# Performance work log

Hardware: AMD Instinct MI355X
Metric: run time of the kernel (lower is better)

## Reference

```python
import jax, jax.numpy as jnp
import numpy as np

ZONEOUT = 0.1
OUT_CHANNELS = 80
REDUCTION_FACTOR = 2


def setup_inputs() -> dict:
    key = jax.random.key(0)
    ks = jax.random.split(key, 7)
    B, H, T, L = 64, 1024, 500, 2
    s = 1.0 / np.sqrt(H)
    return {
        "res_output": jax.random.normal(ks[0], (B, H, T), dtype=jnp.float32),
        "Wih": jax.random.normal(ks[1], (L, 3 * H, H), dtype=jnp.float32) * s,
        "Whh": jax.random.normal(ks[2], (L, 3 * H, H), dtype=jnp.float32) * s,
        "bih": jax.random.normal(ks[3], (L, 3 * H), dtype=jnp.float32) * s,
        "bhh": jax.random.normal(ks[4], (L, 3 * H), dtype=jnp.float32) * s,
        "Wout": jax.random.normal(ks[5], (OUT_CHANNELS * 2, H), dtype=jnp.float32) * s,
        "bout": jax.random.normal(ks[6], (OUT_CHANNELS * 2,), dtype=jnp.float32) * s,
    }


def _gru_cell(x, h, wih, whh, bi, bh):
    # torch.nn.GRUCell math
    gi = x @ wih.T + bi            # (B, 3H)
    gh = h @ whh.T + bh            # (B, 3H)
    i_r, i_z, i_n = jnp.split(gi, 3, axis=-1)
    h_r, h_z, h_n = jnp.split(gh, 3, axis=-1)
    r = jax.nn.sigmoid(i_r + h_r)
    z = jax.nn.sigmoid(i_z + h_z)
    n = jnp.tanh(i_n + r * h_n)
    return (1.0 - z) * n + z * h


def reference(res_output, Wih, Whh, bih, bhh, Wout, bout):
    B, H, T = res_output.shape
    L = Wih.shape[0]
    xs = jnp.transpose(res_output, (2, 0, 1))  # (T, B, H)

    def step(hs, x):
        new_hs = []
        inp = x
        for l in range(L):  # static small layer loop
            h_new = _gru_cell(inp, hs[l], Wih[l], Whh[l], bih[l], bhh[l])
            # eval-mode zoneout: deterministic blend
            h_new = ZONEOUT * hs[l] + (1.0 - ZONEOUT) * h_new
            new_hs.append(h_new)
            inp = h_new
        y = inp @ Wout.T + bout  # (B, 2*out_channels)
        return tuple(new_hs), y

    h0 = tuple(jnp.zeros((B, H), dtype=res_output.dtype) for _ in range(L))
    _, ys = jax.lax.scan(step, h0, xs)  # (T, B, 2*oc)
    ys = ys.reshape(T, B, OUT_CHANNELS, REDUCTION_FACTOR)
    # concat per-step (B, oc, rf) blocks along last dim -> (B, oc, T*rf)
    out = jnp.transpose(ys, (1, 2, 0, 3)).reshape(B, OUT_CHANNELS, T * REDUCTION_FACTOR)
    return out
```

## Files before the change

kernel.cpp:

```cpp
#include <hip/hip_runtime.h>

typedef __attribute__((ext_vector_type(8))) short bhalf8;
typedef __attribute__((ext_vector_type(4))) float floatx4;

#define NSLOTS 502
#define NWG 128
#define BLOCK 768

#define AS1 __attribute__((address_space(1)))
#define AS3 __attribute__((address_space(3)))
#define GLL_COH(g, s)   __builtin_amdgcn_global_load_lds((const AS1 unsigned*)(g), (AS3 unsigned*)(s), 16, 0, 17)
#define GLL_PLAIN(g, s) __builtin_amdgcn_global_load_lds((const AS1 unsigned*)(g), (AS3 unsigned*)(s), 16, 0, 0)

__device__ __forceinline__ unsigned short f2b(float f) {
  unsigned u = __float_as_uint(f);
  return (unsigned short)((u + 0x7FFFu + ((u >> 16) & 1u)) >> 16);
}
__device__ __forceinline__ int cloadi(const int* p) {
  return __hip_atomic_load(p, __ATOMIC_RELAXED, __HIP_MEMORY_SCOPE_AGENT);
}
__device__ __forceinline__ void cstorei(int* p, int v) {
  __hip_atomic_store(p, v, __ATOMIC_RELAXED, __HIP_MEMORY_SCOPE_AGENT);
}
__device__ __forceinline__ void cstore(unsigned long long* p, unsigned long long v) {
  __hip_atomic_store(p, v, __ATOMIC_RELAXED, __HIP_MEMORY_SCOPE_AGENT);
}

__global__ void prep_w(const float* __restrict__ wih, const float* __restrict__ whh,
                       const float* __restrict__ wout,
                       unsigned short* __restrict__ wihb, unsigned short* __restrict__ whhb,
                       unsigned short* __restrict__ woutb) {
  size_t i0 = (size_t)blockIdx.x * blockDim.x + threadIdx.x;
  size_t stride = (size_t)gridDim.x * blockDim.x;
  for (size_t i = i0; i < 6291456u; i += stride) { wihb[i] = f2b(wih[i]); whhb[i] = f2b(whh[i]); }
  for (size_t i = i0; i < 163840u; i += stride) woutb[i] = f2b(wout[i]);
}

__global__ void prep_x(const float* __restrict__ x, unsigned short* __restrict__ xb) {
  __shared__ float tile[32][33];
  int b = blockIdx.z;
  int h0 = blockIdx.y * 32, t0 = blockIdx.x * 32;
  int tx = threadIdx.x, ty = threadIdx.y;
  #pragma unroll
  for (int i = 0; i < 32; i += 8) {
    int t = t0 + tx;
    if (t < 500) tile[ty + i][tx] = x[((size_t)b * 1024 + h0 + ty + i) * 500 + t];
  }
  __syncthreads();
  #pragma unroll
  for (int i = 0; i < 32; i += 8) {
    int t = t0 + ty + i;
    if (t < 500) xb[((size_t)t * 64 + b) * 1024 + h0 + tx] = f2b(tile[tx][ty + i]);
  }
}


__launch_bounds__(BLOCK, 3)
__global__ void gru_main(const unsigned short* __restrict__ xb,
                         const unsigned short* __restrict__ wihb,
                         const unsigned short* __restrict__ whhb,
                         const unsigned short* __restrict__ woutb,
                         const float* __restrict__ bih, const float* __restrict__ bhh,
                         const float* __restrict__ bout,
                         char* __restrict__ wsb, float* __restrict__ out) {
  int* flg = (int*)wsb;
  char* h0p[3] = { wsb + 1024, wsb + 132096, wsb + 263168 };
  char* h1p[2] = { wsb + 394240, wsb + 525312 };

  const int wg = blockIdx.x;
  const int layer = wg >> 6;
  const int sub = wg & 63;
  const int eta = sub >> 5;
  const int c = sub & 31;
  const int n0c = c * 32;
  const int rb = eta * 32;
  const int tid = threadIdx.x;
  const int w = tid >> 6;
  const int l = tid & 63;
  const int l15 = l & 15, l4 = l >> 4;
  const int sd = w / 6;
  const int g = (w % 6) >> 1;
  const int u = w & 1;

  __shared__ __align__(16) char smem[131072];

  const unsigned short* Wsd = (sd ? whhb : wihb) + (size_t)layer * 3145728;
  const unsigned short* wrow = Wsd + (size_t)(g * 1024 + n0c + u * 16 + l15) * 1024 + l4 * 8;

  float bir[3][4], bhr[3][4];
  {
    int j0 = (tid & 7) << 2;
    #pragma unroll
    for (int q = 0; q < 4; ++q)
      #pragma unroll
      for (int gg = 0; gg < 3; ++gg) {
        bir[gg][q] = bih[layer * 3072 + gg * 1024 + n0c + j0 + q];
        bhr[gg][q] = bhh[layer * 3072 + gg * 1024 + n0c + j0 + q];
      }
  }
  float hcr[4] = {0.f, 0.f, 0.f, 0.f};
  int dead = 0;

  for (int s = 0; s < NSLOTS; ++s) {
    if (layer == 0) {
      if (s <= 499) {
        const char* xsrc = (const char*)xb + (size_t)s * 131072 + (size_t)rb * 2048;
        #pragma unroll
        for (int i = 0; i < 6; ++i) {
          int idx = w + i * 12;
          if (idx < 64) {
            int row = idx >> 1, hh = idx & 1;
            GLL_PLAIN(xsrc + row * 2048 + ((hh * 1024 + l * 16) ^ ((row & 7) << 4)),
                      smem + idx * 1024);
          }
        }
        if (w == 0 && !dead) {
          int it = 0;
          for (;;) {
            int f0 = cloadi(&flg[l]);
            int f1 = cloadi(&flg[64 + l]);
            if (__all(f0 >= s && f1 >= s - 1)) break;
            __builtin_amdgcn_s_sleep(1);
            if (++it > 500000) { dead = 1; break; }
          }
        }
        asm volatile("s_waitcnt vmcnt(0)" ::: "memory");
        __builtin_amdgcn_s_barrier();
        __builtin_amdgcn_sched_barrier(0);
        const char* h0src = h0p[(s + 2) % 3] + (size_t)rb * 2048;
        #pragma unroll
        for (int i = 0; i < 6; ++i) {
          int idx = w + i * 12;
          if (idx < 64) {
            int row = idx >> 1, hh = idx & 1;
            GLL_COH(h0src + row * 2048 + ((hh * 1024 + l * 16) ^ ((row & 7) << 4)),
                    smem + 65536 + idx * 1024);
          }
        }
        asm volatile("s_waitcnt vmcnt(0)" ::: "memory");
        __builtin_amdgcn_s_barrier();
        __builtin_amdgcn_sched_barrier(0);
        const char* Ab = smem + sd * 65536;
        floatx4 acc[2];
        acc[0] = (floatx4){0.f, 0.f, 0.f, 0.f};
        acc[1] = (floatx4){0.f, 0.f, 0.f, 0.f};
        #pragma unroll
        for (int ks = 0; ks < 32; ++ks) {
          bhalf8 bb = *(const bhalf8*)(wrow + ks * 32);
          #pragma unroll
          for (int m = 0; m < 2; ++m) {
            int row = m * 16 + l15;
            bhalf8 a = *(const bhalf8*)(Ab + row * 2048 + ((ks * 64 + l4 * 16) ^ ((row & 7) << 4)));
            acc[m] = __builtin_amdgcn_mfma_f32_16x16x32_bf16(a, bb, acc[m], 0, 0, 0);
          }
        }
        __syncthreads();
        float* Gsf = (float*)smem;
        #pragma unroll
        for (int m = 0; m < 2; ++m)
          #pragma unroll
          for (int i = 0; i < 4; ++i)
            Gsf[w * 576 + (m * 16 + l4 * 4 + i) * 18 + l15] = acc[m][i];
        __syncthreads();
        if (tid < 256) {
          int lr = tid >> 3, j0 = (tid & 7) << 2;
          char* hout = h0p[s % 3];
          union { unsigned long long ull; unsigned short us[4]; } pk;
          #pragma unroll
          for (int q = 0; q < 4; ++q) {
            int j = j0 + q, u_ = j >> 4, jj = j & 15;
            float ir  = Gsf[(0 + u_) * 576 + lr * 18 + jj] + bir[0][q];
            float iz  = Gsf[(2 + u_) * 576 + lr * 18 + jj] + bir[1][q];
            float inn = Gsf[(4 + u_) * 576 + lr * 18 + jj] + bir[2][q];
            float hr  = Gsf[(6 + u_) * 576 + lr * 18 + jj] + bhr[0][q];
            float hz  = Gsf[(8 + u_) * 576 + lr * 18 + jj] + bhr[1][q];
            float hn  = Gsf[(10 + u_) * 576 + lr * 18 + jj] + bhr[2][q];
            float rg = 1.f / (1.f + expf(-(ir + hr)));
            float zg = 1.f / (1.f + expf(-(iz + hz)));
            float nc = tanhf(inn + rg * hn);
            float hp = hcr[q];
            float hnew = (1.f - zg) * nc + zg * hp;
            float hzo = 0.1f * hp + 0.9f * hnew;
            hcr[q] = hzo;
            pk.us[q] = f2b(hzo);
          }
          cstore((unsigned long long*)(hout + (size_t)(rb + lr) * 2048 + ((n0c + j0) << 1)), pk.ull);
        }
      }
      __syncthreads();
      if (tid == 0) cstorei(&flg[wg], s + 1);
    } else {
      const bool gemm = (s >= 1 && s <= 500);
      if (s >= 1) {
        if (w == 0 && !dead) {
          int it = 0;
          for (;;) {
            int f0 = cloadi(&flg[l]);
            int f1 = cloadi(&flg[64 + l]);
            if (__all(f0 >= s && f1 >= s)) break;
            __builtin_amdgcn_s_sleep(1);
            if (++it > 500000) { dead = 1; break; }
          }
        }
        __builtin_amdgcn_s_barrier();
        __builtin_amdgcn_sched_barrier(0);
        const char* h0src = h0p[(s + 2) % 3] + (size_t)rb * 2048;
        const char* h1src = h1p[s & 1] + (size_t)rb * 2048;
        if (gemm) {
          #pragma unroll
          for (int i = 0; i < 11; ++i) {
            int idx = w + i * 12;
            if (idx < 128) {
              int pl = idx >> 6, r6 = idx & 63;
              int row = r6 >> 1, hh = r6 & 1;
              GLL_COH((pl ? h1src : h0src) + row * 2048 + ((hh * 1024 + l * 16) ^ ((row & 7) << 4)),
                      smem + pl * 65536 + r6 * 1024);
            }
          }
        } else {
          #pragma unroll
          for (int i = 0; i < 6; ++i) {
            int idx = w + i * 12;
            if (idx < 64) {
              int row = idx >> 1, hh = idx & 1;
              GLL_COH(h1src + row * 2048 + ((hh * 1024 + l * 16) ^ ((row & 7) << 4)),
                      smem + 65536 + idx * 1024);
            }
          }
        }
        asm volatile("s_waitcnt vmcnt(0)" ::: "memory");
        __builtin_amdgcn_s_barrier();
        __builtin_amdgcn_sched_barrier(0);
        floatx4 acc[2];
        acc[0] = (floatx4){0.f, 0.f, 0.f, 0.f};
        acc[1] = (floatx4){0.f, 0.f, 0.f, 0.f};
        if (gemm) {
          const char* Ab = smem + sd * 65536;
          #pragma unroll
          for (int ks = 0; ks < 32; ++ks) {
            bhalf8 bb = *(const bhalf8*)(wrow + ks * 32);
            #pragma unroll
            for (int m = 0; m < 2; ++m) {
              int row = m * 16 + l15;
              bhalf8 a = *(const bhalf8*)(Ab + row * 2048 + ((ks * 64 + l4 * 16) ^ ((row & 7) << 4)));
              acc[m] = __builtin_amdgcn_mfma_f32_16x16x32_bf16(a, bb, acc[m], 0, 0, 0);
            }
          }
        }
        if (s >= 2 && c < 5 && w < 2) {
          int t2 = s - 2;
          #pragma unroll
          for (int nt = 0; nt < 2; ++nt) {
            int col = c * 32 + nt * 16 + l15;
            const unsigned short* brow = woutb + (size_t)col * 1024 + l4 * 8;
            floatx4 accy = (floatx4){0.f, 0.f, 0.f, 0.f};
            #pragma unroll
            for (int ks = 0; ks < 32; ++ks) {
              int row = w * 16 + l15;
              bhalf8 a = *(const bhalf8*)(smem + 65536 + row * 2048 +
                         ((ks * 64 + l4 * 16) ^ ((row & 7) << 4)));
              bhalf8 bb = *(const bhalf8*)(brow + ks * 32);
              accy = __builtin_amdgcn_mfma_f32_16x16x32_bf16(a, bb, accy, 0, 0, 0);
            }
            float bo = bout[col];
            #pragma unroll
            for (int i = 0; i < 4; ++i) {
              int b = rb + w * 16 + l4 * 4 + i;
              out[(size_t)b * 80000 + (size_t)(col >> 1) * 1000 + t2 * 2 + (col & 1)] = accy[i] + bo;
            }
          }
        }
        if (gemm) {
          __syncthreads();
          float* Gsf = (float*)smem;
          #pragma unroll
          for (int m = 0; m < 2; ++m)
            #pragma unroll
            for (int i = 0; i < 4; ++i)
              Gsf[w * 576 + (m * 16 + l4 * 4 + i) * 18 + l15] = acc[m][i];
          __syncthreads();
          if (tid < 256) {
            int lr = tid >> 3, j0 = (tid & 7) << 2;
            char* hout = h1p[(s & 1) ^ 1];
            union { unsigned long long ull; unsigned short us[4]; } pk;
            #pragma unroll
            for (int q = 0; q < 4; ++q) {
              int j = j0 + q, u_ = j >> 4, jj = j & 15;
              float ir  = Gsf[(0 + u_) * 576 + lr * 18 + jj] + bir[0][q];
              float iz  = Gsf[(2 + u_) * 576 + lr * 18 + jj] + bir[1][q];
              float inn = Gsf[(4 + u_) * 576 + lr * 18 + jj] + bir[2][q];
              float hr  = Gsf[(6 + u_) * 576 + lr * 18 + jj] + bhr[0][q];
              float hz  = Gsf[(8 + u_) * 576 + lr * 18 + jj] + bhr[1][q];
              float hn  = Gsf[(10 + u_) * 576 + lr * 18 + jj] + bhr[2][q];
              float rg = 1.f / (1.f + expf(-(ir + hr)));
              float zg = 1.f / (1.f + expf(-(iz + hz)));
              float nc = tanhf(inn + rg * hn);
              float hp = hcr[q];
              float hnew = (1.f - zg) * nc + zg * hp;
              float hzo = 0.1f * hp + 0.9f * hnew;
              hcr[q] = hzo;
              pk.us[q] = f2b(hzo);
            }
            cstore((unsigned long long*)(hout + (size_t)(rb + lr) * 2048 + ((n0c + j0) << 1)), pk.ull);
          }
        }
      }
      __syncthreads();
      if (tid == 0) cstorei(&flg[wg], s + 1);
    }
  }
}

extern "C" void kernel_launch(void* const* d_in, const int* in_sizes, int n_in,
                              void* d_out, int out_size, void* d_ws, size_t ws_size,
                              hipStream_t stream) {
  const float* res  = (const float*)d_in[0];
  const float* Wih  = (const float*)d_in[1];
  const float* Whh  = (const float*)d_in[2];
  const float* bih  = (const float*)d_in[3];
  const float* bhh  = (const float*)d_in[4];
  const float* Wout = (const float*)d_in[5];
  const float* bout = (const float*)d_in[6];
  float* out = (float*)d_out;
  char* ws = (char*)d_ws;
  if (ws_size < 91685888u) return;

  unsigned short* woutb = (unsigned short*)(ws + 656384);
  unsigned short* wihb  = (unsigned short*)(ws + 984064);
  unsigned short* whhb  = (unsigned short*)(ws + 13566976);
  unsigned short* xb    = (unsigned short*)(ws + 26149888);

  hipMemsetAsync(ws, 0, 656384, stream);
  prep_w<<<4096, 256, 0, stream>>>(Wih, Whh, Wout, wihb, whhb, woutb);
  prep_x<<<dim3(16, 32, 64), dim3(32, 8), 0, stream>>>(res, xb);
  gru_main<<<NWG, BLOCK, 0, stream>>>(xb, wihb, whhb, woutb, bih, bhh, bout, ws, out);
}
```

Baseline: 15.89 ms.

## Pin GRU layers to separate XCDs with XCC-local hidden-state exchange

Launches 256 workgroups and uses the hardware XCC ID with an atomic counter to assign 32 workgroups on XCD 0 to layer 0 and 32 on XCD 1 to layer 1, exiting the rest. Each workgroup now handles all 64 batch rows with a K-split across waves. Hidden state stays within one XCD through plain stores and SC0 loads, and layer-0 output crosses to layer 1 through a remote buffer that layer 1 copies locally each step behind an extra flag barrier. The aim is to cut cross-XCD coherent traffic on the serial recurrence. In exchange it adds a copy-and-sync stage, converts Wout from fp32 inline on every step, and depends on enough workgroups landing on XCDs 0 and 1.

```diff
diff --git a/kernel.cpp b/kernel.cpp
--- a/kernel.cpp
+++ b/kernel.cpp
@@ -4,12 +4,11 @@
 typedef __attribute__((ext_vector_type(4))) float floatx4;
 
 #define NSLOTS 502
-#define NWG 128
 #define BLOCK 768
 
 #define AS1 __attribute__((address_space(1)))
 #define AS3 __attribute__((address_space(3)))
-#define GLL_COH(g, s)   __builtin_amdgcn_global_load_lds((const AS1 unsigned*)(g), (AS3 unsigned*)(s), 16, 0, 17)
+#define GLL_SC0(g, s)   __builtin_amdgcn_global_load_lds((const AS1 unsigned*)(g), (AS3 unsigned*)(s), 16, 0, 1)
 #define GLL_PLAIN(g, s) __builtin_amdgcn_global_load_lds((const AS1 unsigned*)(g), (AS3 unsigned*)(s), 16, 0, 0)
 
 __device__ __forceinline__ unsigned short f2b(float f) {
@@ -22,18 +21,18 @@
 __device__ __forceinline__ void cstorei(int* p, int v) {
   __hip_atomic_store(p, v, __ATOMIC_RELAXED, __HIP_MEMORY_SCOPE_AGENT);
 }
-__device__ __forceinline__ void cstore(unsigned long long* p, unsigned long long v) {
+__device__ __forceinline__ unsigned long long cload8(const unsigned long long* p) {
+  return __hip_atomic_load(p, __ATOMIC_RELAXED, __HIP_MEMORY_SCOPE_AGENT);
+}
+__device__ __forceinline__ void cstore8(unsigned long long* p, unsigned long long v) {
   __hip_atomic_store(p, v, __ATOMIC_RELAXED, __HIP_MEMORY_SCOPE_AGENT);
 }
 
 __global__ void prep_w(const float* __restrict__ wih, const float* __restrict__ whh,
-                       const float* __restrict__ wout,
-                       unsigned short* __restrict__ wihb, unsigned short* __restrict__ whhb,
-                       unsigned short* __restrict__ woutb) {
+                       unsigned short* __restrict__ wihb, unsigned short* __restrict__ whhb) {
   size_t i0 = (size_t)blockIdx.x * blockDim.x + threadIdx.x;
   size_t stride = (size_t)gridDim.x * blockDim.x;
   for (size_t i = i0; i < 6291456u; i += stride) { wihb[i] = f2b(wih[i]); whhb[i] = f2b(whh[i]); }
-  for (size_t i = i0; i < 163840u; i += stride) woutb[i] = f2b(wout[i]);
 }
 
 __global__ void prep_x(const float* __restrict__ x, unsigned short* __restrict__ xb) {
@@ -55,37 +54,56 @@
 }
 
 
-__launch_bounds__(BLOCK, 3)
+__launch_bounds__(BLOCK, 1)
 __global__ void gru_main(const unsigned short* __restrict__ xb,
                          const unsigned short* __restrict__ wihb,
                          const unsigned short* __restrict__ whhb,
-                         const unsigned short* __restrict__ woutb,
+                         const float* __restrict__ wout,
                          const float* __restrict__ bih, const float* __restrict__ bhh,
                          const float* __restrict__ bout,
                          char* __restrict__ wsb, float* __restrict__ out) {
-  int* flg = (int*)wsb;
-  char* h0p[3] = { wsb + 1024, wsb + 132096, wsb + 263168 };
-  char* h1p[2] = { wsb + 394240, wsb + 525312 };
-
-  const int wg = blockIdx.x;
-  const int layer = wg >> 6;
-  const int sub = wg & 63;
-  const int eta = sub >> 5;
-  const int c = sub & 31;
-  const int n0c = c * 32;
-  const int rb = eta * 32;
+  int* flgL0rem = (int*)wsb;
+  int* flgL1rem = (int*)(wsb + 128);
+  int* flgCopy  = (int*)(wsb + 384);
+  int* xcdcnt   = (int*)(wsb + 512);
+  char* h0rem  = wsb + 1024;
+  char* h1loc  = wsb + 263168;
+  char* h0loc0 = wsb + 525312;
+  char* h0loc1 = wsb + 787456;
+
   const int tid = threadIdx.x;
   const int w = tid >> 6;
   const int l = tid & 63;
   const int l15 = l & 15, l4 = l >> 4;
-  const int sd = w / 6;
-  const int g = (w % 6) >> 1;
-  const int u = w & 1;
+  const int g = w >> 2;
+  const int u = (w >> 1) & 1;
+  const int kh = w & 1;
 
   __shared__ __align__(16) char smem[131072];
-
-  const unsigned short* Wsd = (sd ? whhb : wihb) + (size_t)layer * 3145728;
-  const unsigned short* wrow = Wsd + (size_t)(g * 1024 + n0c + u * 16 + l15) * 1024 + l4 * 8;
+  __shared__ int role_sh;
+
+  unsigned xcc;
+  asm volatile("s_getreg_b32 %0, hwreg(HW_REG_XCC_ID)" : "=s"(xcc));
+  xcc &= 7u;
+  if (tid == 0) {
+    int rank = __hip_atomic_fetch_add(&xcdcnt[xcc], 1, __ATOMIC_RELAXED, __HIP_MEMORY_SCOPE_AGENT);
+    int role = -1;
+    if (xcc == 0 && rank < 32) role = rank;
+    else if (xcc == 1 && rank < 32) role = 32 + rank;
+    role_sh = role;
+  }
+  __syncthreads();
+  const int role = role_sh;
+  if (role < 0) return;
+
+  const int layer = (role < 32) ? 0 : 1;
+  const int c = (layer == 0) ? role : role - 32;
+  const int n0c = c * 32;
+
+  const unsigned short* wrowA = wihb + (size_t)layer * 3145728 +
+      (size_t)(g * 1024 + n0c + u * 16 + l15) * 1024 + kh * 512 + l4 * 8;
+  const unsigned short* wrowB = whhb + (size_t)layer * 3145728 +
+      (size_t)(g * 1024 + n0c + u * 16 + l15) * 1024 + kh * 512 + l4 * 8;
 
   float bir[3][4], bhr[3][4];
   {
@@ -101,80 +119,92 @@
   float hcr[4] = {0.f, 0.f, 0.f, 0.f};
   int dead = 0;
 
-  for (int s = 0; s < NSLOTS; ++s) {
-    if (layer == 0) {
+  auto gather = [&](const char* src, int sc0) {
+    #pragma unroll
+    for (int i = 0; i < 11; ++i) {
+      int idx = w + i * 12;
+      if (idx < 128) {
+        int row = idx >> 1, hh = idx & 1;
+        const char* ga = src + row * 2048 + ((hh * 1024 + l * 16) ^ ((row & 7) << 4));
+        if (sc0) GLL_SC0(ga, smem + idx * 1024); else GLL_PLAIN(ga, smem + idx * 1024);
+      }
+    }
+  };
+  auto gemm = [&](const unsigned short* wrow, floatx4* acc) {
+    #pragma unroll
+    for (int ks = 0; ks < 16; ++ks) {
+      bhalf8 bb = *(const bhalf8*)(wrow + ks * 32);
+      #pragma unroll
+      for (int m = 0; m < 4; ++m) {
+        int row = m * 16 + l15;
+        bhalf8 a = *(const bhalf8*)(smem + row * 2048 +
+                   ((kh * 1024 + ks * 64 + l4 * 16) ^ ((row & 7) << 4)));
+        acc[m] = __builtin_amdgcn_mfma_f32_16x16x32_bf16(a, bb, acc[m], 0, 0, 0);
+      }
+    }
+  };
+  auto dumpGs = [&](floatx4* acc, int sideofs) {
+    float* Gsf = (float*)smem;
+    #pragma unroll
+    for (int m = 0; m < 4; ++m)
+      #pragma unroll
+      for (int i = 0; i < 4; ++i)
+        Gsf[(sideofs + w) * 1088 + (m * 16 + l4 * 4 + i) * 17 + l15] = acc[m][i];
+  };
+
+  if (layer == 0) {
+    for (int s = 0; s < NSLOTS; ++s) {
       if (s <= 499) {
-        const char* xsrc = (const char*)xb + (size_t)s * 131072 + (size_t)rb * 2048;
-        #pragma unroll
-        for (int i = 0; i < 6; ++i) {
-          int idx = w + i * 12;
-          if (idx < 64) {
-            int row = idx >> 1, hh = idx & 1;
-            GLL_PLAIN(xsrc + row * 2048 + ((hh * 1024 + l * 16) ^ ((row & 7) << 4)),
-                      smem + idx * 1024);
-          }
-        }
+        gather((const char*)xb + (size_t)s * 131072, 0);
         if (w == 0 && !dead) {
           int it = 0;
           for (;;) {
-            int f0 = cloadi(&flg[l]);
-            int f1 = cloadi(&flg[64 + l]);
-            if (__all(f0 >= s && f1 >= s - 1)) break;
-            __builtin_amdgcn_s_sleep(1);
-            if (++it > 500000) { dead = 1; break; }
+            int ok = (l < 32) ? (cloadi(&flgL0rem[l]) >= s)
+                              : (cloadi(&flgL1rem[l - 32]) >= s - 1);
+            if (__all(ok)) break;
+            __builtin_amdgcn_s_sleep(2);
+            if (++it > 300000) { dead = 1; break; }
           }
         }
         asm volatile("s_waitcnt vmcnt(0)" ::: "memory");
         __builtin_amdgcn_s_barrier();
         __builtin_amdgcn_sched_barrier(0);
-        const char* h0src = h0p[(s + 2) % 3] + (size_t)rb * 2048;
+
+        floatx4 accI[4], accH[4];
         #pragma unroll
-        for (int i = 0; i < 6; ++i) {
-          int idx = w + i * 12;
-          if (idx < 64) {
-            int row = idx >> 1, hh = idx & 1;
-            GLL_COH(h0src + row * 2048 + ((hh * 1024 + l * 16) ^ ((row & 7) << 4)),
-                    smem + 65536 + idx * 1024);
-          }
-        }
+        for (int m = 0; m < 4; ++m) {
+          accI[m] = (floatx4){0.f, 0.f, 0.f, 0.f};
+          accH[m] = (floatx4){0.f, 0.f, 0.f, 0.f};
+        }
+        gemm(wrowA, accI);
+        __syncthreads();
+        gather(h0loc0 + (size_t)((s + 1) & 1) * 131072, 1);
         asm volatile("s_waitcnt vmcnt(0)" ::: "memory");
         __builtin_amdgcn_s_barrier();
         __builtin_amdgcn_sched_barrier(0);
-        const char* Ab = smem + sd * 65536;
-        floatx4 acc[2];
-        acc[0] = (floatx4){0.f, 0.f, 0.f, 0.f};
-        acc[1] = (floatx4){0.f, 0.f, 0.f, 0.f};
-        #pragma unroll
-        for (int ks = 0; ks < 32; ++ks) {
-          bhalf8 bb = *(const bhalf8*)(wrow + ks * 32);
-          #pragma unroll
-          for (int m = 0; m < 2; ++m) {
-            int row = m * 16 + l15;
-            bhalf8 a = *(const bhalf8*)(Ab + row * 2048 + ((ks * 64 + l4 * 16) ^ ((row & 7) << 4)));
-            acc[m] = __builtin_amdgcn_mfma_f32_16x16x32_bf16(a, bb, acc[m], 0, 0, 0);
-          }
-        }
+        gemm(wrowB, accH);
+        __syncthreads();
+        dumpGs(accI, 0);
+        dumpGs(accH, 12);
         __syncthreads();
         float* Gsf = (float*)smem;
-        #pragma unroll
-        for (int m = 0; m < 2; ++m)
-          #pragma unroll
-          for (int i = 0; i < 4; ++i)
-            Gsf[w * 576 + (m * 16 + l4 * 4 + i) * 18 + l15] = acc[m][i];
-        __syncthreads();
-        if (tid < 256) {
-          int lr = tid >> 3, j0 = (tid & 7) << 2;
-          char* hout = h0p[s % 3];
+        if (tid < 512) {
+          int b = tid >> 3, j0 = (tid & 7) << 2, u_ = j0 >> 4;
+          char* houtL = h0loc0 + (size_t)(s & 1) * 131072;
+          char* houtR = h0rem  + (size_t)(s & 1) * 131072;
           union { unsigned long long ull; unsigned short us[4]; } pk;
           #pragma unroll
           for (int q = 0; q < 4; ++q) {
-            int j = j0 + q, u_ = j >> 4, jj = j & 15;
-            float ir  = Gsf[(0 + u_) * 576 + lr * 18 + jj] + bir[0][q];
-            float iz  = Gsf[(2 + u_) * 576 + lr * 18 + jj] + bir[1][q];
-            float inn = Gsf[(4 + u_) * 576 + lr * 18 + jj] + bir[2][q];
-            float hr  = Gsf[(6 + u_) * 576 + lr * 18 + jj] + bhr[0][q];
-            float hz  = Gsf[(8 + u_) * 576 + lr * 18 + jj] + bhr[1][q];
-            float hn  = Gsf[(10 + u_) * 576 + lr * 18 + jj] + bhr[2][q];
+            int jj = (j0 + q) & 15;
+            float gi[3], gh[3];
+            #pragma unroll
+            for (int gg = 0; gg < 3; ++gg) {
+              int pw = gg * 4 + u_ * 2;
+              gi[gg] = Gsf[pw * 1088 + b * 17 + jj] + Gsf[(pw + 1) * 1088 + b * 17 + jj];
+              gh[gg] = Gsf[(12 + pw) * 1088 + b * 17 + jj] + Gsf[(12 + pw + 1) * 1088 + b * 17 + jj];
+            }
+            float ir = gi[0] + bir[0][q], iz = gi[1] + bir[1][q], inn = gi[2] + bir[2][q];
+            float hr = gh[0] + bhr[0][q], hz = gh[1] + bhr[1][q], hn = gh[2] + bhr[2][q];
             float rg = 1.f / (1.f + expf(-(ir + hr)));
             float zg = 1.f / (1.f + expf(-(iz + hz)));
             float nc = tanhf(inn + rg * hn);
@@ -184,114 +214,112 @@
             hcr[q] = hzo;
             pk.us[q] = f2b(hzo);
           }
-          cstore((unsigned long long*)(hout + (size_t)(rb + lr) * 2048 + ((n0c + j0) << 1)), pk.ull);
+          size_t off = (size_t)b * 2048 + ((n0c + j0) << 1);
+          *(volatile unsigned long long*)(houtL + off) = pk.ull;
+          cstore8((unsigned long long*)(houtR + off), pk.ull);
         }
       }
       __syncthreads();
-      if (tid == 0) cstorei(&flg[wg], s + 1);
-    } else {
-      const bool gemm = (s >= 1 && s <= 500);
+      if (tid == 0) cstorei(&flgL0rem[c], s + 1);
+    }
+  } else {
+    for (int s = 0; s < NSLOTS; ++s) {
       if (s >= 1) {
+        const bool doGemm = (s <= 500);
         if (w == 0 && !dead) {
           int it = 0;
           for (;;) {
-            int f0 = cloadi(&flg[l]);
-            int f1 = cloadi(&flg[64 + l]);
-            if (__all(f0 >= s && f1 >= s)) break;
-            __builtin_amdgcn_s_sleep(1);
-            if (++it > 500000) { dead = 1; break; }
+            int ok = (l < 32) ? (cloadi(&flgL0rem[l]) >= s)
+                              : (cloadi(&flgL1rem[l - 32]) >= s);
+            if (__all(ok)) break;
+            __builtin_amdgcn_s_sleep(2);
+            if (++it > 300000) { dead = 1; break; }
           }
         }
         __builtin_amdgcn_s_barrier();
         __builtin_amdgcn_sched_barrier(0);
-        const char* h0src = h0p[(s + 2) % 3] + (size_t)rb * 2048;
-        const char* h1src = h1p[s & 1] + (size_t)rb * 2048;
-        if (gemm) {
-          #pragma unroll
-          for (int i = 0; i < 11; ++i) {
-            int idx = w + i * 12;
-            if (idx < 128) {
-              int pl = idx >> 6, r6 = idx & 63;
-              int row = r6 >> 1, hh = r6 & 1;
-              GLL_COH((pl ? h1src : h0src) + row * 2048 + ((hh * 1024 + l * 16) ^ ((row & 7) << 4)),
-                      smem + pl * 65536 + r6 * 1024);
+        floatx4 accI[4], accH[4];
+        #pragma unroll
+        for (int m = 0; m < 4; ++m) {
+          accI[m] = (floatx4){0.f, 0.f, 0.f, 0.f};
+          accH[m] = (floatx4){0.f, 0.f, 0.f, 0.f};
+        }
+        if (doGemm) {
+          if (w == 0 && !dead) {
+            const char* src = h0rem + (size_t)((s + 1) & 1) * 131072;
+            char* dst = h0loc1;
+            int row = 2 * c + (l >> 5), off = (l & 31) * 64;
+            #pragma unroll
+            for (int k = 0; k < 8; ++k) {
+              unsigned long long v = cload8((const unsigned long long*)(src + (size_t)row * 2048 + off + k * 8));
+              *(volatile unsigned long long*)(dst + (size_t)row * 2048 + off + k * 8) = v;
             }
-          }
-        } else {
-          #pragma unroll
-          for (int i = 0; i < 6; ++i) {
-            int idx = w + i * 12;
-            if (idx < 64) {
-              int row = idx >> 1, hh = idx & 1;
-              GLL_COH(h1src + row * 2048 + ((hh * 1024 + l * 16) ^ ((row & 7) << 4)),
-                      smem + 65536 + idx * 1024);
+            asm volatile("s_waitcnt vmcnt(0)" ::: "memory");
+            if (l == 0) cstorei(&flgCopy[c], s + 1);
+            int it = 0;
+            while (!__all(cloadi(&flgCopy[l & 31]) >= s + 1)) {
+              __builtin_amdgcn_s_sleep(1);
+              if (++it > 300000) { dead = 1; break; }
             }
           }
-        }
+          __syncthreads();
+          gather(h0loc1, 1);
+          asm volatile("s_waitcnt vmcnt(0)" ::: "memory");
+          __builtin_amdgcn_s_barrier();
+          __builtin_amdgcn_sched_barrier(0);
+          gemm(wrowA, accI);
+          __syncthreads();
+        }
+        gather(h1loc + (size_t)(s & 1) * 131072, 1);
         asm volatile("s_waitcnt vmcnt(0)" ::: "memory");
         __builtin_amdgcn_s_barrier();
         __builtin_amdgcn_sched_barrier(0);
-        floatx4 acc[2];
-        acc[0] = (floatx4){0.f, 0.f, 0.f, 0.f};
-        acc[1] = (floatx4){0.f, 0.f, 0.f, 0.f};
-        if (gemm) {
-          const char* Ab = smem + sd * 65536;
+        if (doGemm) gemm(wrowB, accH);
+        if (s >= 2 && c < 20 && w < 2) {
+          int tile = c * 2 + w, bt = tile / 10, ct = tile % 10;
+          int col = ct * 16 + l15;
+          const float* wr = wout + (size_t)col * 1024 + l4 * 8;
+          floatx4 accy = (floatx4){0.f, 0.f, 0.f, 0.f};
           #pragma unroll
           for (int ks = 0; ks < 32; ++ks) {
-            bhalf8 bb = *(const bhalf8*)(wrow + ks * 32);
+            union { bhalf8 v; unsigned short us[8]; } bw;
             #pragma unroll
-            for (int m = 0; m < 2; ++m) {
-              int row = m * 16 + l15;
-              bhalf8 a = *(const bhalf8*)(Ab + row * 2048 + ((ks * 64 + l4 * 16) ^ ((row & 7) << 4)));
-              acc[m] = __builtin_amdgcn_mfma_f32_16x16x32_bf16(a, bb, acc[m], 0, 0, 0);
-            }
-          }
-        }
-        if (s >= 2 && c < 5 && w < 2) {
+            for (int e = 0; e < 8; ++e) bw.us[e] = f2b(wr[ks * 32 + e]);
+            int row = bt * 16 + l15;
+            bhalf8 a = *(const bhalf8*)(smem + row * 2048 +
+                       ((ks * 64 + l4 * 16) ^ ((row & 7) << 4)));
+            accy = __builtin_amdgcn_mfma_f32_16x16x32_bf16(a, bw.v, accy, 0, 0, 0);
+          }
+          float bo = bout[col];
           int t2 = s - 2;
           #pragma unroll
-          for (int nt = 0; nt < 2; ++nt) {
-            int col = c * 32 + nt * 16 + l15;
-            const unsigned short* brow = woutb + (size_t)col * 1024 + l4 * 8;
-            floatx4 accy = (floatx4){0.f, 0.f, 0.f, 0.f};
-            #pragma unroll
-            for (int ks = 0; ks < 32; ++ks) {
-              int row = w * 16 + l15;
-              bhalf8 a = *(const bhalf8*)(smem + 65536 + row * 2048 +
-                         ((ks * 64 + l4 * 16) ^ ((row & 7) << 4)));
-              bhalf8 bb = *(const bhalf8*)(brow + ks * 32);
-              accy = __builtin_amdgcn_mfma_f32_16x16x32_bf16(a, bb, accy, 0, 0, 0);
-            }
-            float bo = bout[col];
-            #pragma unroll
-            for (int i = 0; i < 4; ++i) {
-              int b = rb + w * 16 + l4 * 4 + i;
-              out[(size_t)b * 80000 + (size_t)(col >> 1) * 1000 + t2 * 2 + (col & 1)] = accy[i] + bo;
-            }
-          }
-        }
-        if (gemm) {
+          for (int i = 0; i < 4; ++i) {
+            int b = bt * 16 + l4 * 4 + i;
+            out[(size_t)b * 80000 + (size_t)(col >> 1) * 1000 + t2 * 2 + (col & 1)] = accy[i] + bo;
+          }
+        }
+        if (doGemm) {
+          __syncthreads();
+          dumpGs(accI, 0);
+          dumpGs(accH, 12);
           __syncthreads();
           float* Gsf = (float*)smem;
-          #pragma unroll
-          for (int m = 0; m < 2; ++m)
-            #pragma unroll
-            for (int i = 0; i < 4; ++i)
-              Gsf[w * 576 + (m * 16 + l4 * 4 + i) * 18 + l15] = acc[m][i];
-          __syncthreads();
-          if (tid < 256) {
-            int lr = tid >> 3, j0 = (tid & 7) << 2;
-            char* hout = h1p[(s & 1) ^ 1];
+          if (tid < 512) {
+            int b = tid >> 3, j0 = (tid & 7) << 2, u_ = j0 >> 4;
+            char* hout = h1loc + (size_t)((s + 1) & 1) * 131072;
             union { unsigned long long ull; unsigned short us[4]; } pk;
             #pragma unroll
             for (int q = 0; q < 4; ++q) {
-              int j = j0 + q, u_ = j >> 4, jj = j & 15;
-              float ir  = Gsf[(0 + u_) * 576 + lr * 18 + jj] + bir[0][q];
-              float iz  = Gsf[(2 + u_) * 576 + lr * 18 + jj] + bir[1][q];
-              float inn = Gsf[(4 + u_) * 576 + lr * 18 + jj] + bir[2][q];
-              float hr  = Gsf[(6 + u_) * 576 + lr * 18 + jj] + bhr[0][q];
-              float hz  = Gsf[(8 + u_) * 576 + lr * 18 + jj] + bhr[1][q];
-              float hn  = Gsf[(10 + u_) * 576 + lr * 18 + jj] + bhr[2][q];
+              int jj = (j0 + q) & 15;
+              float gi[3], gh[3];
+              #pragma unroll
+              for (int gg = 0; gg < 3; ++gg) {
+                int pw = gg * 4 + u_ * 2;
+                gi[gg] = Gsf[pw * 1088 + b * 17 + jj] + Gsf[(pw + 1) * 1088 + b * 17 + jj];
+                gh[gg] = Gsf[(12 + pw) * 1088 + b * 17 + jj] + Gsf[(12 + pw + 1) * 1088 + b * 17 + jj];
+              }
+              float ir = gi[0] + bir[0][q], iz = gi[1] + bir[1][q], inn = gi[2] + bir[2][q];
+              float hr = gh[0] + bhr[0][q], hz = gh[1] + bhr[1][q], hn = gh[2] + bhr[2][q];
               float rg = 1.f / (1.f + expf(-(ir + hr)));
               float zg = 1.f / (1.f + expf(-(iz + hz)));
               float nc = tanhf(inn + rg * hn);
@@ -301,12 +329,12 @@
               hcr[q] = hzo;
               pk.us[q] = f2b(hzo);
             }
-            cstore((unsigned long long*)(hout + (size_t)(rb + lr) * 2048 + ((n0c + j0) << 1)), pk.ull);
+            *(volatile unsigned long long*)(hout + (size_t)b * 2048 + ((n0c + j0) << 1)) = pk.ull;
           }
         }
       }
       __syncthreads();
-      if (tid == 0) cstorei(&flg[wg], s + 1);
+      if (tid == 0) cstorei(&flgL1rem[c], s + 1);
     }
   }
 }
@@ -323,15 +351,14 @@
   const float* bout = (const float*)d_in[6];
   float* out = (float*)d_out;
   char* ws = (char*)d_ws;
-  if (ws_size < 91685888u) return;
-
-  unsigned short* woutb = (unsigned short*)(ws + 656384);
-  unsigned short* wihb  = (unsigned short*)(ws + 984064);
-  unsigned short* whhb  = (unsigned short*)(ws + 13566976);
-  unsigned short* xb    = (unsigned short*)(ws + 26149888);
-
-  hipMemsetAsync(ws, 0, 656384, stream);
-  prep_w<<<4096, 256, 0, stream>>>(Wih, Whh, Wout, wihb, whhb, woutb);
+  if (ws_size < 91620352u) return;
+
+  unsigned short* wihb = (unsigned short*)(ws + 918528);
+  unsigned short* whhb = (unsigned short*)(ws + 13501440);
+  unsigned short* xb   = (unsigned short*)(ws + 26084352);
+
+  hipMemsetAsync(ws, 0, 918528, stream);
+  prep_w<<<4096, 256, 0, stream>>>(Wih, Whh, wihb, whhb);
   prep_x<<<dim3(16, 32, 64), dim3(32, 8), 0, stream>>>(res, xb);
-  gru_main<<<NWG, BLOCK, 0, stream>>>(xb, wihb, whhb, woutb, bih, bhh, bout, ws, out);
-}
+  gru_main<<<256, BLOCK, 0, stream>>>(xb, wihb, whhb, Wout, bih, bhh, bout, ws, out);
+}
```

Result: slower. 23.32 ms (+46.7%).
